# Performance work log

Hardware: AMD Instinct MI355X
Metric: run time of the kernel (lower is better)

Reference implementation:

```python
import jax, jax.numpy as jnp
import numpy as np

EPS = 1e-6
R_DEPTH = 12   # CONFIG['max_recursion_depth']
STACK = 48     # CONFIG['stack_size']
GB, CG, CC = 0.8, 2.0, 0.25  # graph_bias_scale, context_gate_strength, commitment_cost


def _g(k, shape, s=0.05):
    return (jax.random.normal(k, shape) * s).astype(jnp.float32)


def setup_inputs():
    D, V, B, S = 128, 16384, 32, 128
    NS, NM = 64, 128
    ks = iter(jax.random.split(jax.random.key(0), 40))
    return {
        "input_ids": jax.random.randint(next(ks), (B, S), 0, V),
        "prev_syn_idx": jax.random.randint(next(ks), (B,), 0, NS),
        "prev_sem_idx": jax.random.randint(next(ks), (B,), 0, NM),
        "emb_mag": _g(next(ks), (V, D), 1.0),
        "emb_phase": _g(next(ks), (V, D), 1.0),
        "cell_Wr": _g(next(ks), (D, D)), "cell_Wi": _g(next(ks), (D, D)),
        "norm_scale": jnp.ones((D,), jnp.float32),
        "norm_shift": jnp.zeros((D,), jnp.float32),
        "modrelu_b": jnp.zeros((D,), jnp.float32),
        "qWr": _g(next(ks), (D, D)), "qWi": _g(next(ks), (D, D)),
        "kWr": _g(next(ks), (D, D)), "kWi": _g(next(ks), (D, D)),
        "vWr": _g(next(ks), (D, D)), "vWi": _g(next(ks), (D, D)),
        "oWr": _g(next(ks), (D, D)), "oWi": _g(next(ks), (D, D)),
        "halt_W": _g(next(ks), (2 * D, 1)),
        "halt_b": jnp.full((1,), -2.0, jnp.float32),  # nn.init.constant_(halt_linear.bias, -2.0)
        "stk_W": _g(next(ks), (2 * D, 3)), "stk_b": jnp.zeros((3,), jnp.float32),
        "cb_syn": _g(next(ks), (64, 2 * D), 1.0),
        "cb_sem": _g(next(ks), (128, 2 * D), 1.0),
        "ctxsyn_W": _g(next(ks), (2 * D, NS)), "ctxsyn_b": jnp.zeros((NS,), jnp.float32),
        "ctxsem_W": _g(next(ks), (2 * D, NM)), "ctxsem_b": jnp.zeros((NM,), jnp.float32),
        "adj_syn": _g(next(ks), (NS, NS), 1.0),
        "adj_sem": _g(next(ks), (NM, NM), 1.0),
        "gate_W": _g(next(ks), (4 * D, D)), "gate_b": jnp.zeros((D,), jnp.float32),
        "dec_W": _g(next(ks), (2 * D, V)), "dec_b": jnp.zeros((V,), jnp.float32),
    }


def _forward(fl, input_ids, prev_syn_idx, prev_sem_idx):
    (emb_mag, emb_phase, cell_Wr, cell_Wi, norm_scale, norm_shift, modrelu_b,
     qWr, qWi, kWr, kWi, vWr, vWi, oWr, oWi, halt_W, halt_b, stk_W, stk_b,
     cb_syn, cb_sem, ctxsyn_W, ctxsyn_b, ctxsem_W, ctxsem_b, adj_syn, adj_sem,
     gate_W, gate_b, dec_W, dec_b) = fl
    B = input_ids.shape[0]
    D = emb_mag.shape[1]
    sg = jax.lax.stop_gradient

    def clin(r, i, Wr, Wi):  # ComplexLinear (no bias)
        return r @ Wr - i @ Wi, i @ Wr + r @ Wi

    def cell(zr, zi):  # AdaptiveRecursiveCell
        r, i = clin(zr, zi, cell_Wr, cell_Wi)
        # ComplexLayerNorm (torch.var is unbiased -> ddof=1)
        mag = jnp.sqrt(r * r + i * i) + EPS
        mean = mag.mean(-1, keepdims=True)
        var = jnp.var(mag, axis=-1, ddof=1, keepdims=True)
        nm = (mag - mean) / jnp.sqrt(var + EPS) * norm_scale + norm_shift
        r, i = nm * r / mag, nm * i / mag  # cos/sin of original phase
        # ModReLU
        n = jnp.sqrt(r * r + i * i) + EPS
        s = jax.nn.relu(n + modrelu_b) / n
        r, i = r * s, i * s
        # MultiHeadComplexAttention: source computes Q,K but out = V -> o_proj(v_proj(z))
        vr, vi = clin(r, i, vWr, vWi)
        r, i = clin(vr, vi, oWr, oWi)
        zf = jnp.concatenate([r, i], -1)
        halt = jax.nn.sigmoid(zf @ halt_W + halt_b)          # [B,1]
        ctrl = jax.nn.softmax(zf @ stk_W + stk_b, axis=-1)   # [B,3]
        return r, i, halt, ctrl

    def stack_step(zr, zi, mem, ptr, ctrl):  # DifferentiableStack
        push, pop, noop = ctrl[:, 0:1], ctrl[:, 1:2], ctrl[:, 2:3]
        pu, pd = jnp.roll(ptr, 1, axis=1), jnp.roll(ptr, -1, axis=1)
        nptr = push * pu + pop * pd + noop * ptr
        nptr = nptr / (nptr.sum(1, keepdims=True) + EPS)
        zf = jnp.concatenate([zr, zi], -1)
        wm = (push * pu)[:, :, None]                          # write mask [B,STACK,1]
        mem = wm * zf[:, None, :] + mem * (1.0 - wm)
        read = (mem * nptr[:, :, None]).sum(1)                # [B,2D]
        return read[:, :D], read[:, D:], mem, nptr

    def gres(zr, zi, sr, si):  # GatedResidual, g_c = g + i*g
        g = jax.nn.sigmoid(jnp.concatenate([zr, zi, sr, si], -1) @ gate_W + gate_b)
        return ((1.0 - g) * zr + g * zi + g * (sr - si),
                (1.0 - g) * zi - g * zr + g * (si + sr))

    def vq(zr, zi, cb, adj, cW, cbias, pidx):  # ContextAwareDualVQ.vq_step (eval mode)
        zf = jnp.concatenate([zr, zi], -1)                    # [B,2D]
        d = (zf * zf).sum(1, keepdims=True) + (cb * cb).sum(1) - 2.0 * zf @ cb.T
        d = d - GB * jax.nn.sigmoid(adj[pidx]) - CG * jax.nn.softmax(zf @ cW + cbias, -1)
        idx = jnp.argmin(d, axis=1)
        zq = cb[idx]
        loss = jnp.mean((sg(zq) - zf) ** 2) + CC * jnp.mean((zq - sg(zf)) ** 2)
        return zf + sg(zq - zf), loss, idx                    # STE

    def step(carry, ids_t):
        mem, ptr, psyn, psem, lacc = carry
        r, th = emb_mag[ids_t], emb_phase[ids_t]              # embed
        zr, zi = r * jnp.cos(th), r * jnp.sin(th)
        rem = jnp.ones((B, 1), zr.dtype)
        accr = jnp.zeros_like(zr); acci = jnp.zeros_like(zi)
        slr = jnp.zeros_like(zr); sli = jnp.zeros_like(zi)
        for n in range(R_DEPTH):  # ACT recursion, halting-weighted accumulation
            pr, pi, halt, ctrl = cell(zr, zi)
            rr, ri, mem, ptr = stack_step(pr, pi, mem, ptr, ctrl)
            zr, zi = gres(pr, pi, rr, ri)
            w = rem if n == R_DEPTH - 1 else rem * halt
            accr, acci = accr + w * zr, acci + w * zi
            rem = rem * (1.0 - halt)
            slr, sli = slr + zr / R_DEPTH, sli + zi / R_DEPTH
        zqs, ls, isyn = vq(accr, acci, cb_syn, adj_syn, ctxsyn_W, ctxsyn_b, psyn)
        zqm, lm, isem = vq(slr, sli, cb_sem, adj_sem, ctxsem_W, ctxsem_b, psem)
        logits = 0.5 * (zqs + zqm) @ dec_W + dec_b            # decoder: Linear(2D, V)
        return (mem, ptr, isyn, isem, lacc + ls + lm), logits

    mem0 = jnp.zeros((B, STACK, 2 * D), jnp.float32)
    ptr0 = jnp.zeros((B, STACK), jnp.float32).at[:, 0].set(1.0)
    carry0 = (mem0, ptr0, prev_syn_idx, prev_sem_idx, jnp.zeros((), jnp.float32))
    (_, _, _, _, vq_loss), logits = jax.lax.scan(step, carry0, input_ids.T)
    return jnp.transpose(logits, (1, 0, 2)), vq_loss          # [B,S,V], scalar


def reference(input_ids, prev_syn_idx, prev_sem_idx, emb_mag, emb_phase, cell_Wr, cell_Wi, norm_scale, norm_shift, modrelu_b, qWr, qWi, kWr, kWi, vWr, vWi, oWr, oWi, halt_W, halt_b, stk_W, stk_b, cb_syn, cb_sem, ctxsyn_W, ctxsyn_b, ctxsem_W, ctxsem_b, adj_syn, adj_sem, gate_W, gate_b, dec_W, dec_b):
    fl = (emb_mag, emb_phase, cell_Wr, cell_Wi, norm_scale, norm_shift, modrelu_b,
          qWr, qWi, kWr, kWi, vWr, vWi, oWr, oWi, halt_W, halt_b, stk_W, stk_b,
          cb_syn, cb_sem, ctxsyn_W, ctxsyn_b, ctxsem_W, ctxsem_b, adj_syn, adj_sem,
          gate_W, gate_b, dec_W, dec_b)
    return _forward(fl, input_ids, prev_syn_idx, prev_sem_idx)
```

## Files before the change

### kernel.cpp

```cpp
#include <hip/hip_runtime.h>
#include <math.h>

#define D 128
#define D2 256
#define STK 48
#define SEQ 128
#define BATCH 32
#define RDPT 12
#define NSYN 64
#define NSEM 128
#define VOC 16384
#define EPSF 1e-6f
#define GB_C 0.8f
#define CG_C 2.0f

struct RParams {
  const int* input_ids;
  const int* prev_syn;
  const int* prev_sem;
  const float* emb_mag;
  const float* emb_phase;
  const float* cell_Wr;
  const float* cell_Wi;
  const float* norm_scale;
  const float* norm_shift;
  const float* modrelu_b;
  const float* VOr;
  const float* VOi;
  const float* halt_W;
  const float* halt_b;
  const float* stk_W;
  const float* stk_b;
  const float* cb_syn;
  const float* cb_sem;
  const float* ctxsyn_W;
  const float* ctxsyn_b;
  const float* ctxsem_W;
  const float* ctxsem_b;
  const float* gate_W;
  const float* gate_b;
  const float* cbT_syn;
  const float* cbT_sem;
  const float* cnrm_syn;
  const float* cnrm_sem;
  const float* gbsig_syn;
  const float* gbsig_sem;
  float* X;
  float* lossp;
};

__device__ __forceinline__ float waveAllSum(float v) {
  #pragma unroll
  for (int m = 32; m; m >>= 1) v += __shfl_xor(v, m);
  return v;
}

__global__ __launch_bounds__(512, 2) void recur_kernel(RParams p) {
  __shared__ float2 VO2[D * D];
  __shared__ float partr[512], parti[512];
  __shared__ alignas(16) float xr_[D], xi_[D], cr_[D], ci_[D];
  __shared__ float rAiA[D2], marr[D];
  __shared__ alignas(16) float zfc[D2], rd_[D2];
  __shared__ alignas(16) float acc2[D2], sl2[D2];
  __shared__ float zqs[D2];
  __shared__ float sptr[STK];
  __shared__ alignas(16) float nptrs[STK], wms[STK];
  __shared__ float scal[16];
  __shared__ int icb[2];
  __shared__ int ids[SEQ];

  const int tid = threadIdx.x;
  const int b = blockIdx.x;
  const int wv = tid >> 6;
  const int l = tid & 63;
  const int j = tid & 127;
  const int kq = tid >> 7;
  const int k0 = kq * 32;

  float cwr[32], cwi[32];
  #pragma unroll
  for (int kk = 0; kk < 32; ++kk) {
    cwr[kk] = p.cell_Wr[(size_t)(k0 + kk) * D + j];
    cwi[kk] = p.cell_Wi[(size_t)(k0 + kk) * D + j];
  }
  float gw[128];
  #pragma unroll
  for (int kk = 0; kk < 128; ++kk)
    gw[kk] = p.gate_W[(size_t)(kq * 128 + kk) * D + j];
  {
    const float4* r4p = (const float4*)p.VOr;
    const float4* i4p = (const float4*)p.VOi;
    float4* dst = (float4*)VO2;
    for (int e = tid; e < D * D / 4; e += 512) {
      float4 r4 = r4p[e];
      float4 i4 = i4p[e];
      float4 lo, hi;
      lo.x = r4.x; lo.y = i4.x; lo.z = r4.y; lo.w = i4.y;
      hi.x = r4.z; hi.y = i4.z; hi.z = r4.w; hi.w = i4.w;
      dst[e * 2 + 0] = lo;
      dst[e * 2 + 1] = hi;
    }
  }
  float snsR = 0.f, nshR = 0.f, smbR = 0.f, sgbR = 0.f;
  if (tid < D) {
    snsR = p.norm_scale[tid];
    nshR = p.norm_shift[tid];
    smbR = p.modrelu_b[tid];
    sgbR = p.gate_b[tid];
  }
  float hwr0 = 0.f, hwr1 = 0.f, hwr2 = 0.f, hwr3 = 0.f;
  if (wv == 0) {
    hwr0 = p.halt_W[l]; hwr1 = p.halt_W[l + 64];
    hwr2 = p.halt_W[l + 128]; hwr3 = p.halt_W[l + 192];
  } else if (wv < 4) {
    const int c = wv - 1;
    hwr0 = p.stk_W[l * 3 + c]; hwr1 = p.stk_W[(l + 64) * 3 + c];
    hwr2 = p.stk_W[(l + 128) * 3 + c]; hwr3 = p.stk_W[(l + 192) * 3 + c];
  }
  if (tid < SEQ) ids[tid] = p.input_ids[(size_t)b * SEQ + tid];
  if (tid < STK) sptr[tid] = (tid == 0) ? 1.f : 0.f;
  if (tid == 0) { icb[0] = p.prev_syn[b]; icb[1] = p.prev_sem[b]; }
  const float hb = p.halt_b[0];
  const float sb0 = p.stk_b[0], sb1 = p.stk_b[1], sb2 = p.stk_b[2];

  float memv[24];
  #pragma unroll
  for (int q = 0; q < 24; ++q) memv[q] = 0.f;
  const int mdl = tid & 255, mjh = tid >> 8;
  float lossAcc = 0.f;
  __syncthreads();

  for (int t = 0; t < SEQ; ++t) {
    const int id = ids[t];
    if (tid < D) {
      float m = p.emb_mag[(size_t)id * D + tid];
      float ph = p.emb_phase[(size_t)id * D + tid];
      float sv, cv;
      sincosf(ph, &sv, &cv);
      xr_[tid] = m * cv;
      xi_[tid] = m * sv;
    }
    float remv = 1.f;
    float accR = 0.f, accI = 0.f, slR = 0.f, slI = 0.f;
    __syncthreads();

    for (int n = 0; n < RDPT; ++n) {
      {
        const float4* x4r = (const float4*)(&xr_[k0]);
        const float4* x4i = (const float4*)(&xi_[k0]);
        float a0 = 0.f, a1 = 0.f, a2 = 0.f, a3 = 0.f;
        #pragma unroll
        for (int q = 0; q < 8; ++q) {
          float4 xa = x4r[q];
          float4 xb = x4i[q];
          a0 = fmaf(xa.x, cwr[q*4+0], a0); a0 = fmaf(-xb.x, cwi[q*4+0], a0);
          a1 = fmaf(xb.x, cwr[q*4+0], a1); a1 = fmaf(xa.x, cwi[q*4+0], a1);
          a2 = fmaf(xa.y, cwr[q*4+1], a2); a2 = fmaf(-xb.y, cwi[q*4+1], a2);
          a3 = fmaf(xb.y, cwr[q*4+1], a3); a3 = fmaf(xa.y, cwi[q*4+1], a3);
          a0 = fmaf(xa.z, cwr[q*4+2], a0); a0 = fmaf(-xb.z, cwi[q*4+2], a0);
          a1 = fmaf(xb.z, cwr[q*4+2], a1); a1 = fmaf(xa.z, cwi[q*4+2], a1);
          a2 = fmaf(xa.w, cwr[q*4+3], a2); a2 = fmaf(-xb.w, cwi[q*4+3], a2);
          a3 = fmaf(xb.w, cwr[q*4+3], a3); a3 = fmaf(xa.w, cwi[q*4+3], a3);
        }
        partr[tid] = a0 + a2;
        parti[tid] = a1 + a3;
      }
      __syncthreads();
      if (tid < D) {
        float rr = partr[tid] + partr[tid + 128] + partr[tid + 256] + partr[tid + 384];
        float ii = parti[tid] + parti[tid + 128] + parti[tid + 256] + parti[tid + 384];
        rAiA[tid] = rr;
        rAiA[tid + 128] = ii;
        marr[tid] = sqrtf(rr * rr + ii * ii) + EPSF;
      }
      __syncthreads();
      if (tid < 64) {
        float m0 = marr[l], m1 = marr[l + 64];
        float s = waveAllSum(m0 + m1);
        float mean = s * (1.f / D);
        float d0 = m0 - mean, d1 = m1 - mean;
        float v = waveAllSum(d0 * d0 + d1 * d1);
        if (l == 0) {
          scal[1] = mean;
          scal[2] = rsqrtf(v * (1.f / (D - 1)) + EPSF);
        }
      }
      __syncthreads();
      if (tid < D) {
        float m = marr[tid];
        float nm = (m - scal[1]) * scal[2] * snsR + nshR;
        float r_ = nm * rAiA[tid] / m;
        float i_ = nm * rAiA[tid + 128] / m;
        float nn = sqrtf(r_ * r_ + i_ * i_) + EPSF;
        float sc = fmaxf(nn + smbR, 0.f) / nn;
        cr_[tid] = r_ * sc;
        ci_[tid] = i_ * sc;
      }
      __syncthreads();
      {
        const float4* c4r = (const float4*)(&cr_[k0]);
        const float4* c4i = (const float4*)(&ci_[k0]);
        float a0 = 0.f, a1 = 0.f, a2 = 0.f, a3 = 0.f;
        #pragma unroll
        for (int q = 0; q < 8; ++q) {
          float4 xa = c4r[q];
          float4 xb = c4i[q];
          const int kb = k0 + q * 4;
          float2 w0 = VO2[(size_t)(kb + 0) * D + j];
          float2 w1 = VO2[(size_t)(kb + 1) * D + j];
          float2 w2 = VO2[(size_t)(kb + 2) * D + j];
          float2 w3 = VO2[(size_t)(kb + 3) * D + j];
          a0 = fmaf(xa.x, w0.x, a0); a0 = fmaf(-xb.x, w0.y, a0);
          a1 = fmaf(xb.x, w0.x, a1); a1 = fmaf(xa.x, w0.y, a1);
          a2 = fmaf(xa.y, w1.x, a2); a2 = fmaf(-xb.y, w1.y, a2);
          a3 = fmaf(xb.y, w1.x, a3); a3 = fmaf(xa.y, w1.y, a3);
          a0 = fmaf(xa.z, w2.x, a0); a0 = fmaf(-xb.z, w2.y, a0);
          a1 = fmaf(xb.z, w2.x, a1); a1 = fmaf(xa.z, w2.y, a1);
          a2 = fmaf(xa.w, w3.x, a2); a2 = fmaf(-xb.w, w3.y, a2);
          a3 = fmaf(xb.w, w3.x, a3); a3 = fmaf(xa.w, w3.y, a3);
        }
        partr[tid] = a0 + a2;
        parti[tid] = a1 + a3;
      }
      __syncthreads();
      if (tid < D) {
        zfc[tid] = partr[tid] + partr[tid + 128] + partr[tid + 256] + partr[tid + 384];
        zfc[tid + 128] = parti[tid] + parti[tid + 128] + parti[tid + 256] + parti[tid + 384];
      }
      __syncthreads();
      if (tid < 256) {
        float s = zfc[l] * hwr0 + zfc[l + 64] * hwr1 +
                  zfc[l + 128] * hwr2 + zfc[l + 192] * hwr3;
        s = waveAllSum(s);
        if (l == 0) scal[4 + wv] = s;
      }
      __syncthreads();
      if (tid < 64) {
        float halt = 1.f / (1.f + expf(-(scal[4] + hb)));
        float e0 = scal[5] + sb0, e1 = scal[6] + sb1, e2 = scal[7] + sb2;
        float mx = fmaxf(e0, fmaxf(e1, e2));
        float x0 = expf(e0 - mx), x1 = expf(e1 - mx), x2 = expf(e2 - mx);
        float sm = x0 + x1 + x2;
        float push = x0 / sm, pop = x1 / sm, noop = x2 / sm;
        float wgt = (n == RDPT - 1) ? remv : remv * halt;
        if (l == 0) scal[3] = wgt;
        remv = remv * (1.f - halt);
        float pj = 0.f, pu = 0.f, pd = 0.f;
        if (l < STK) {
          pj = sptr[l];
          pu = sptr[(l + STK - 1) % STK];
          pd = sptr[(l + 1) % STK];
        }
        float np_ = push * pu + pop * pd + noop * pj;
        float wm_ = push * pu;
        float ssum = waveAllSum((l < STK) ? np_ : 0.f);
        float inv = 1.f / (ssum + EPSF);
        if (l < STK) {
          np_ *= inv;
          nptrs[l] = np_;
          sptr[l] = np_;
          wms[l] = wm_;
        }
      }
      __syncthreads();
      {
        const float4* wm4 = (const float4*)wms;
        const float4* np4 = (const float4*)nptrs;
        float zfd = zfc[mdl];
        float accA = 0.f, accB = 0.f;
        #pragma unroll
        for (int m4 = 0; m4 < 6; ++m4) {
          float4 wmv = wm4[mjh * 6 + m4];
          float4 npv = np4[mjh * 6 + m4];
          const int base = m4 * 4;
          memv[base + 0] = wmv.x * zfd + memv[base + 0] * (1.f - wmv.x);
          accA = fmaf(memv[base + 0], npv.x, accA);
          memv[base + 1] = wmv.y * zfd + memv[base + 1] * (1.f - wmv.y);
          accB = fmaf(memv[base + 1], npv.y, accB);
          memv[base + 2] = wmv.z * zfd + memv[base + 2] * (1.f - wmv.z);
          accA = fmaf(memv[base + 2], npv.z, accA);
          memv[base + 3] = wmv.w * zfd + memv[base + 3] * (1.f - wmv.w);
          accB = fmaf(memv[base + 3], npv.w, accB);
        }
        partr[tid] = accA + accB;
      }
      __syncthreads();
      if (tid < D2) rd_[tid] = partr[tid] + partr[tid + 256];
      __syncthreads();
      {
        const float4* src4 = (kq < 2) ? (const float4*)(&zfc[kq * 128])
                                      : (const float4*)(&rd_[(kq - 2) * 128]);
        float g0 = 0.f, g1 = 0.f, g2 = 0.f, g3 = 0.f;
        #pragma unroll
        for (int q = 0; q < 32; ++q) {
          float4 xv = src4[q];
          g0 = fmaf(xv.x, gw[q * 4 + 0], g0);
          g1 = fmaf(xv.y, gw[q * 4 + 1], g1);
          g2 = fmaf(xv.z, gw[q * 4 + 2], g2);
          g3 = fmaf(xv.w, gw[q * 4 + 3], g3);
        }
        partr[tid] = (g0 + g1) + (g2 + g3);
      }
      __syncthreads();
      if (tid < D) {
        float g = partr[tid] + partr[tid + 128] + partr[tid + 256] +
                  partr[tid + 384] + sgbR;
        g = 1.f / (1.f + expf(-g));
        float pr_ = zfc[tid], pi_ = zfc[tid + 128];
        float rr_ = rd_[tid], ri_ = rd_[tid + 128];
        float nzr = (1.f - g) * pr_ + g * pi_ + g * (rr_ - ri_);
        float nzi = (1.f - g) * pi_ - g * pr_ + g * (ri_ + rr_);
        xr_[tid] = nzr;
        xi_[tid] = nzi;
        float wgt = scal[3];
        accR += wgt * nzr;
        accI += wgt * nzi;
        slR += nzr * (1.f / RDPT);
        slI += nzi * (1.f / RDPT);
      }
      __syncthreads();
    }

    if (tid < D) {
      acc2[tid] = accR; acc2[tid + 128] = accI;
      sl2[tid] = slR;  sl2[tid + 128] = slI;
    }
    __syncthreads();

    {
      const int c = tid & 63, ch = tid >> 6;
      const int kb = ch * 32;
      const float* cb = p.cbT_syn + (size_t)kb * 64 + c;
      const float* cw = p.ctxsyn_W + (size_t)kb * 64 + c;
      const float4* a4 = (const float4*)(&acc2[kb]);
      float d0 = 0.f, d1 = 0.f, e0 = 0.f, e1 = 0.f;
      #pragma unroll
      for (int q = 0; q < 8; ++q) {
        float4 zv = a4[q];
        d0 = fmaf(cb[(size_t)(q * 4 + 0) * 64], zv.x, d0);
        e0 = fmaf(cw[(size_t)(q * 4 + 0) * 64], zv.x, e0);
        d1 = fmaf(cb[(size_t)(q * 4 + 1) * 64], zv.y, d1);
        e1 = fmaf(cw[(size_t)(q * 4 + 1) * 64], zv.y, e1);
        d0 = fmaf(cb[(size_t)(q * 4 + 2) * 64], zv.z, d0);
        e0 = fmaf(cw[(size_t)(q * 4 + 2) * 64], zv.z, e0);
        d1 = fmaf(cb[(size_t)(q * 4 + 3) * 64], zv.w, d1);
        e1 = fmaf(cw[(size_t)(q * 4 + 3) * 64], zv.w, e1);
      }
      partr[ch * 64 + c] = d0 + d1;
      parti[ch * 64 + c] = e0 + e1;
    }
    __syncthreads();
    if (tid < 64) {
      float dot = 0.f, e = p.ctxsyn_b[l];
      #pragma unroll
      for (int ch = 0; ch < 8; ++ch) {
        dot += partr[ch * 64 + l];
        e += parti[ch * 64 + l];
      }
      float d = p.cnrm_syn[l] - 2.f * dot;
      float m = e;
      #pragma unroll
      for (int mm = 32; mm; mm >>= 1) m = fmaxf(m, __shfl_xor(m, mm));
      float ex = expf(e - m);
      float s = waveAllSum(ex);
      const int pidx = icb[0];
      float score = d - p.gbsig_syn[(size_t)pidx * 64 + l] - CG_C * (ex / s);
      float bv = score; int bi = l;
      #pragma unroll
      for (int mm = 32; mm; mm >>= 1) {
        float ov = __shfl_xor(bv, mm); int oi = __shfl_xor(bi, mm);
        if (ov < bv || (ov == bv && oi < bi)) { bv = ov; bi = oi; }
      }
      if (l == 0) icb[0] = bi;
    }
    __syncthreads();
    if (tid < D2) {
      const int idx = icb[0];
      float zqv = p.cb_syn[(size_t)idx * D2 + tid];
      float df = zqv - acc2[tid];
      lossAcc += df * df;
      zqs[tid] = zqv;
    }
    {
      const int c = tid & 127, ch = tid >> 7;
      const int kb = ch * 64;
      const float* cb = p.cbT_sem + (size_t)kb * 128 + c;
      const float* cw = p.ctxsem_W + (size_t)kb * 128 + c;
      const float4* a4 = (const float4*)(&sl2[kb]);
      float d0 = 0.f, d1 = 0.f, e0 = 0.f, e1 = 0.f;
      #pragma unroll
      for (int q = 0; q < 16; ++q) {
        float4 zv = a4[q];
        d0 = fmaf(cb[(size_t)(q * 4 + 0) * 128], zv.x, d0);
        e0 = fmaf(cw[(size_t)(q * 4 + 0) * 128], zv.x, e0);
        d1 = fmaf(cb[(size_t)(q * 4 + 1) * 128], zv.y, d1);
        e1 = fmaf(cw[(size_t)(q * 4 + 1) * 128], zv.y, e1);
        d0 = fmaf(cb[(size_t)(q * 4 + 2) * 128], zv.z, d0);
        e0 = fmaf(cw[(size_t)(q * 4 + 2) * 128], zv.z, e0);
        d1 = fmaf(cb[(size_t)(q * 4 + 3) * 128], zv.w, d1);
        e1 = fmaf(cw[(size_t)(q * 4 + 3) * 128], zv.w, e1);
      }
      partr[ch * 128 + c] = d0 + d1;
      parti[ch * 128 + c] = e0 + e1;
    }
    __syncthreads();
    if (tid < 64) {
      float dot0 = 0.f, e0 = p.ctxsem_b[l];
      float dot1 = 0.f, e1 = p.ctxsem_b[l + 64];
      #pragma unroll
      for (int ch = 0; ch < 4; ++ch) {
        dot0 += partr[ch * 128 + l];       e0 += parti[ch * 128 + l];
        dot1 += partr[ch * 128 + l + 64];  e1 += parti[ch * 128 + l + 64];
      }
      float d0 = p.cnrm_sem[l] - 2.f * dot0;
      float d1 = p.cnrm_sem[l + 64] - 2.f * dot1;
      float m = fmaxf(e0, e1);
      #pragma unroll
      for (int mm = 32; mm; mm >>= 1) m = fmaxf(m, __shfl_xor(m, mm));
      float x0 = expf(e0 - m), x1 = expf(e1 - m);
      float s = waveAllSum(x0 + x1);
      const int pidx = icb[1];
      float s0 = d0 - p.gbsig_sem[(size_t)pidx * 128 + l] - CG_C * (x0 / s);
      float s1 = d1 - p.gbsig_sem[(size_t)pidx * 128 + l + 64] - CG_C * (x1 / s);
      float bv = s0; int bi = l;
      if (s1 < bv) { bv = s1; bi = l + 64; }
      #pragma unroll
      for (int mm = 32; mm; mm >>= 1) {
        float ov = __shfl_xor(bv, mm); int oi = __shfl_xor(bi, mm);
        if (ov < bv || (ov == bv && oi < bi)) { bv = ov; bi = oi; }
      }
      if (l == 0) icb[1] = bi;
    }
    __syncthreads();
    if (tid < D2) {
      const int idx = icb[1];
      float zqv = p.cb_sem[(size_t)idx * D2 + tid];
      float df = zqv - sl2[tid];
      lossAcc += df * df;
      p.X[(size_t)(b * SEQ + t) * D2 + tid] = 0.5f * (zqs[tid] + zqv);
    }
    __syncthreads();
  }

  partr[tid] = lossAcc;
  __syncthreads();
  if (tid < 256) partr[tid] += partr[tid + 256];
  __syncthreads();
  if (tid < 128) partr[tid] += partr[tid + 128];
  __syncthreads();
  if (tid < 64) {
    float v = partr[tid] + partr[tid + 64];
    v = waveAllSum(v);
    if (tid == 0) p.lossp[b] = v;
  }
}

__global__ __launch_bounds__(256) void voprod_kernel(const float* __restrict__ vr,
                                                     const float* __restrict__ vi,
                                                     const float* __restrict__ orr,
                                                     const float* __restrict__ oii,
                                                     float* __restrict__ VOr,
                                                     float* __restrict__ VOi) {
  __shared__ float a_r[D], a_i[D];
  const int k = blockIdx.x;
  const int tid = threadIdx.x;
  if (tid < D) { a_r[tid] = vr[k * D + tid]; a_i[tid] = vi[k * D + tid]; }
  __syncthreads();
  const int m = tid & 127;
  const int half = tid >> 7;
  float acc = 0.f;
  if (half == 0) {
    #pragma unroll 8
    for (int jj = 0; jj < D; ++jj)
      acc += a_r[jj] * orr[jj * D + m] - a_i[jj] * oii[jj * D + m];
    VOr[k * D + m] = acc;
  } else {
    #pragma unroll 8
    for (int jj = 0; jj < D; ++jj)
      acc += a_r[jj] * oii[jj * D + m] + a_i[jj] * orr[jj * D + m];
    VOi[k * D + m] = acc;
  }
}

__global__ void vqprep_kernel(const float* __restrict__ cb_syn,
                              const float* __restrict__ cb_sem,
                              const float* __restrict__ adj_syn,
                              const float* __restrict__ adj_sem,
                              float* __restrict__ cbT_syn,
                              float* __restrict__ cbT_sem,
                              float* __restrict__ cnrm_syn,
                              float* __restrict__ cnrm_sem,
                              float* __restrict__ gbsig_syn,
                              float* __restrict__ gbsig_sem) {
  const int tid = blockIdx.x * 256 + threadIdx.x;
  const int nt = gridDim.x * 256;
  for (int e = tid; e < NSYN * D2; e += nt) {
    int c = e / D2, k = e % D2;
    cbT_syn[k * NSYN + c] = cb_syn[e];
  }
  for (int e = tid; e < NSEM * D2; e += nt) {
    int c = e / D2, k = e % D2;
    cbT_sem[k * NSEM + c] = cb_sem[e];
  }
  for (int c = tid; c < NSYN; c += nt) {
    float s = 0.f;
    for (int k = 0; k < D2; ++k) { float v = cb_syn[c * D2 + k]; s += v * v; }
    cnrm_syn[c] = s;
  }
  for (int c = tid; c < NSEM; c += nt) {
    float s = 0.f;
    for (int k = 0; k < D2; ++k) { float v = cb_sem[c * D2 + k]; s += v * v; }
    cnrm_sem[c] = s;
  }
  for (int e = tid; e < NSYN * NSYN; e += nt)
    gbsig_syn[e] = GB_C / (1.f + expf(-adj_syn[e]));
  for (int e = tid; e < NSEM * NSEM; e += nt)
    gbsig_sem[e] = GB_C / (1.f + expf(-adj_sem[e]));
}

__global__ __launch_bounds__(256) void dec_kernel(const float* __restrict__ X,
                                                  const float* __restrict__ W,
                                                  const float* __restrict__ bias,
                                                  float* __restrict__ out) {
  __shared__ float A[32][D2];
  const int tid = threadIdx.x;
  const int bx = blockIdx.x;
  const int by = blockIdx.y;
  const float* xr = X + (size_t)by * 32 * D2;
  #pragma unroll
  for (int s = 0; s < 32; ++s) A[s][tid] = xr[s * D2 + tid];
  __syncthreads();
  const int ty = tid >> 5, tx = tid & 31;
  const int col0 = bx * 128 + tx * 4;
  const int r0 = ty * 4;
  float acc[4][4];
  #pragma unroll
  for (int r = 0; r < 4; ++r) {
    acc[r][0] = 0.f; acc[r][1] = 0.f; acc[r][2] = 0.f; acc[r][3] = 0.f;
  }
  const float* wp = W + col0;
  for (int k = 0; k < D2; k += 4) {
    float4 w0 = *(const float4*)(wp + (size_t)(k + 0) * VOC);
    float4 w1 = *(const float4*)(wp + (size_t)(k + 1) * VOC);
    float4 w2 = *(const float4*)(wp + (size_t)(k + 2) * VOC);
    float4 w3 = *(const float4*)(wp + (size_t)(k + 3) * VOC);
    #pragma unroll
    for (int r = 0; r < 4; ++r) {
      float4 a = *(const float4*)&A[r0 + r][k];
      acc[r][0] += a.x * w0.x + a.y * w1.x + a.z * w2.x + a.w * w3.x;
      acc[r][1] += a.x * w0.y + a.y * w1.y + a.z * w2.y + a.w * w3.y;
      acc[r][2] += a.x * w0.z + a.y * w1.z + a.z * w2.z + a.w * w3.z;
      acc[r][3] += a.x * w0.w + a.y * w1.w + a.z * w2.w + a.w * w3.w;
    }
  }
  float4 bv = *(const float4*)(bias + col0);
  #pragma unroll
  for (int r = 0; r < 4; ++r) {
    float4 o;
    o.x = acc[r][0] + bv.x; o.y = acc[r][1] + bv.y;
    o.z = acc[r][2] + bv.z; o.w = acc[r][3] + bv.w;
    *(float4*)(out + (size_t)(by * 32 + r0 + r) * VOC + col0) = o;
  }
}

__global__ void loss_kernel(const float* __restrict__ lp, float* __restrict__ out) {
  int l = threadIdx.x;
  float v = (l < BATCH) ? lp[l] : 0.f;
  #pragma unroll
  for (int off = 32; off; off >>= 1) v += __shfl_down(v, off);
  if (l == 0) out[0] = v * (1.25f / 8192.f);
}

extern "C" void kernel_launch(void* const* d_in, const int* in_sizes, int n_in,
                              void* d_out, int out_size, void* d_ws,
                              size_t ws_size, hipStream_t stream) {
  float* ws = (float*)d_ws;
  float* X = ws;
  float* lossp = X + 1048576;
  float* VOr = lossp + 64;
  float* VOi = VOr + 16384;
  float* cbT_syn = VOi + 16384;
  float* cbT_sem = cbT_syn + 16384;
  float* cnrm_syn = cbT_sem + 32768;
  float* cnrm_sem = cnrm_syn + 64;
  float* gbsig_syn = cnrm_sem + 128;
  float* gbsig_sem = gbsig_syn + 4096;

  RParams p;
  p.input_ids  = (const int*)d_in[0];
  p.prev_syn   = (const int*)d_in[1];
  p.prev_sem   = (const int*)d_in[2];
  p.emb_mag    = (const float*)d_in[3];
  p.emb_phase  = (const float*)d_in[4];
  p.cell_Wr    = (const float*)d_in[5];
  p.cell_Wi    = (const float*)d_in[6];
  p.norm_scale = (const float*)d_in[7];
  p.norm_shift = (const float*)d_in[8];
  p.modrelu_b  = (const float*)d_in[9];
  p.VOr        = VOr;
  p.VOi        = VOi;
  p.halt_W     = (const float*)d_in[18];
  p.halt_b     = (const float*)d_in[19];
  p.stk_W      = (const float*)d_in[20];
  p.stk_b      = (const float*)d_in[21];
  p.cb_syn     = (const float*)d_in[22];
  p.cb_sem     = (const float*)d_in[23];
  p.ctxsyn_W   = (const float*)d_in[24];
  p.ctxsyn_b   = (const float*)d_in[25];
  p.ctxsem_W   = (const float*)d_in[26];
  p.ctxsem_b   = (const float*)d_in[27];
  p.gate_W     = (const float*)d_in[30];
  p.gate_b     = (const float*)d_in[31];
  const float* dec_W = (const float*)d_in[32];
  const float* dec_b = (const float*)d_in[33];
  p.cbT_syn = cbT_syn;
  p.cbT_sem = cbT_sem;
  p.cnrm_syn = cnrm_syn;
  p.cnrm_sem = cnrm_sem;
  p.gbsig_syn = gbsig_syn;
  p.gbsig_sem = gbsig_sem;
  p.X = X;
  p.lossp = lossp;

  float* out = (float*)d_out;

  voprod_kernel<<<D, 256, 0, stream>>>((const float*)d_in[14], (const float*)d_in[15],
                                       (const float*)d_in[16], (const float*)d_in[17],
                                       VOr, VOi);
  vqprep_kernel<<<64, 256, 0, stream>>>((const float*)d_in[22], (const float*)d_in[23],
                                        (const float*)d_in[28], (const float*)d_in[29],
                                        cbT_syn, cbT_sem, cnrm_syn, cnrm_sem,
                                        gbsig_syn, gbsig_sem);
  recur_kernel<<<BATCH, 512, 0, stream>>>(p);
  dec_kernel<<<dim3(VOC / 128, BATCH * SEQ / 32), 256, 0, stream>>>(X, dec_W,
                                                                    dec_b, out);
  loss_kernel<<<1, 64, 0, stream>>>(lossp, out + (size_t)BATCH * SEQ * VOC);
}
```

Before: 16.74 ms.

## Merge reduction and normalization stages to cut barriers in recurrent loop

Inside the 12-step inner recursion, the cell-output reduction, magnitude statistics and modReLU normalization are folded into one wave-0 stage. The halt and stack projections are now computed by a single wave from shared-memory copies of the weights, which removes several __syncthreads per iteration. The VO weight tile is repacked as float4 pairs so each thread does half as many LDS reads. Embedding rows for the next token are prefetched during the tail of the current step. The cost is that more serial work lands on one wave, so other waves sit idle for longer, and the extra shared arrays increase LDS use.

```diff
diff --git a/kernel.cpp b/kernel.cpp
--- a/kernel.cpp
+++ b/kernel.cpp
@@ -56,22 +56,23 @@
 }
 
 __global__ __launch_bounds__(512, 2) void recur_kernel(RParams p) {
-  __shared__ float2 VO2[D * D];
+  __shared__ float4 VO4[(D / 2) * D];
   __shared__ float partr[512], parti[512];
   __shared__ alignas(16) float xr_[D], xi_[D], cr_[D], ci_[D];
-  __shared__ float rAiA[D2], marr[D];
   __shared__ alignas(16) float zfc[D2], rd_[D2];
   __shared__ alignas(16) float acc2[D2], sl2[D2];
   __shared__ float zqs[D2];
   __shared__ float sptr[STK];
   __shared__ alignas(16) float nptrs[STK], wms[STK];
+  __shared__ float sns_s[D], nsh_s[D], smb_s[D];
+  __shared__ float hW_s[D2];
+  __shared__ float stW_s[D2 * 3];
   __shared__ float scal[16];
   __shared__ int icb[2];
   __shared__ int ids[SEQ];
 
   const int tid = threadIdx.x;
   const int b = blockIdx.x;
-  const int wv = tid >> 6;
   const int l = tid & 63;
   const int j = tid & 127;
   const int kq = tid >> 7;
@@ -87,36 +88,24 @@
   #pragma unroll
   for (int kk = 0; kk < 128; ++kk)
     gw[kk] = p.gate_W[(size_t)(kq * 128 + kk) * D + j];
-  {
-    const float4* r4p = (const float4*)p.VOr;
-    const float4* i4p = (const float4*)p.VOi;
-    float4* dst = (float4*)VO2;
-    for (int e = tid; e < D * D / 4; e += 512) {
-      float4 r4 = r4p[e];
-      float4 i4 = i4p[e];
-      float4 lo, hi;
-      lo.x = r4.x; lo.y = i4.x; lo.z = r4.y; lo.w = i4.y;
-      hi.x = r4.z; hi.y = i4.z; hi.z = r4.w; hi.w = i4.w;
-      dst[e * 2 + 0] = lo;
-      dst[e * 2 + 1] = hi;
-    }
-  }
-  float snsR = 0.f, nshR = 0.f, smbR = 0.f, sgbR = 0.f;
+  for (int e = tid; e < (D / 2) * D; e += 512) {
+    const int kp = e >> 7;
+    const int jj = e & 127;
+    float4 w;
+    w.x = p.VOr[(size_t)(2 * kp) * D + jj];
+    w.y = p.VOi[(size_t)(2 * kp) * D + jj];
+    w.z = p.VOr[(size_t)(2 * kp + 1) * D + jj];
+    w.w = p.VOi[(size_t)(2 * kp + 1) * D + jj];
+    VO4[e] = w;
+  }
   if (tid < D) {
-    snsR = p.norm_scale[tid];
-    nshR = p.norm_shift[tid];
-    smbR = p.modrelu_b[tid];
-    sgbR = p.gate_b[tid];
-  }
-  float hwr0 = 0.f, hwr1 = 0.f, hwr2 = 0.f, hwr3 = 0.f;
-  if (wv == 0) {
-    hwr0 = p.halt_W[l]; hwr1 = p.halt_W[l + 64];
-    hwr2 = p.halt_W[l + 128]; hwr3 = p.halt_W[l + 192];
-  } else if (wv < 4) {
-    const int c = wv - 1;
-    hwr0 = p.stk_W[l * 3 + c]; hwr1 = p.stk_W[(l + 64) * 3 + c];
-    hwr2 = p.stk_W[(l + 128) * 3 + c]; hwr3 = p.stk_W[(l + 192) * 3 + c];
-  }
+    sns_s[tid] = p.norm_scale[tid];
+    nsh_s[tid] = p.norm_shift[tid];
+    smb_s[tid] = p.modrelu_b[tid];
+  }
+  const float sgbR = (tid < D) ? p.gate_b[tid] : 0.f;
+  if (tid < D2) hW_s[tid] = p.halt_W[tid];
+  for (int e = tid; e < D2 * 3; e += 512) stW_s[e] = p.stk_W[e];
   if (tid < SEQ) ids[tid] = p.input_ids[(size_t)b * SEQ + tid];
   if (tid < STK) sptr[tid] = (tid == 0) ? 1.f : 0.f;
   if (tid == 0) { icb[0] = p.prev_syn[b]; icb[1] = p.prev_sem[b]; }
@@ -128,20 +117,25 @@
   for (int q = 0; q < 24; ++q) memv[q] = 0.f;
   const int mdl = tid & 255, mjh = tid >> 8;
   float lossAcc = 0.f;
+  float remv = 1.f;
+  float mNxt = 0.f, pNxt = 0.f;
   __syncthreads();
 
+  if (tid < D) {
+    const int id0 = ids[0];
+    mNxt = p.emb_mag[(size_t)id0 * D + tid];
+    pNxt = p.emb_phase[(size_t)id0 * D + tid];
+  }
+
   for (int t = 0; t < SEQ; ++t) {
-    const int id = ids[t];
     if (tid < D) {
-      float m = p.emb_mag[(size_t)id * D + tid];
-      float ph = p.emb_phase[(size_t)id * D + tid];
       float sv, cv;
-      sincosf(ph, &sv, &cv);
-      xr_[tid] = m * cv;
-      xi_[tid] = m * sv;
-    }
-    float remv = 1.f;
+      sincosf(pNxt, &sv, &cv);
+      xr_[tid] = mNxt * cv;
+      xi_[tid] = mNxt * sv;
+    }
     float accR = 0.f, accI = 0.f, slR = 0.f, slI = 0.f;
+    if (tid < 64) remv = 1.f;
     __syncthreads();
 
     for (int n = 0; n < RDPT; ++n) {
@@ -166,78 +160,80 @@
         parti[tid] = a1 + a3;
       }
       __syncthreads();
-      if (tid < D) {
-        float rr = partr[tid] + partr[tid + 128] + partr[tid + 256] + partr[tid + 384];
-        float ii = parti[tid] + parti[tid + 128] + parti[tid + 256] + parti[tid + 384];
-        rAiA[tid] = rr;
-        rAiA[tid + 128] = ii;
-        marr[tid] = sqrtf(rr * rr + ii * ii) + EPSF;
-      }
-      __syncthreads();
       if (tid < 64) {
-        float m0 = marr[l], m1 = marr[l + 64];
-        float s = waveAllSum(m0 + m1);
-        float mean = s * (1.f / D);
-        float d0 = m0 - mean, d1 = m1 - mean;
-        float v = waveAllSum(d0 * d0 + d1 * d1);
-        if (l == 0) {
-          scal[1] = mean;
-          scal[2] = rsqrtf(v * (1.f / (D - 1)) + EPSF);
-        }
-      }
-      __syncthreads();
-      if (tid < D) {
-        float m = marr[tid];
-        float nm = (m - scal[1]) * scal[2] * snsR + nshR;
-        float r_ = nm * rAiA[tid] / m;
-        float i_ = nm * rAiA[tid + 128] / m;
-        float nn = sqrtf(r_ * r_ + i_ * i_) + EPSF;
-        float sc = fmaxf(nn + smbR, 0.f) / nn;
-        cr_[tid] = r_ * sc;
-        ci_[tid] = i_ * sc;
+        float rr0 = 0.f, ii0 = 0.f, rr1 = 0.f, ii1 = 0.f;
+        #pragma unroll
+        for (int q = 0; q < 4; ++q) {
+          rr0 += partr[l + q * 128];       ii0 += parti[l + q * 128];
+          rr1 += partr[l + 64 + q * 128];  ii1 += parti[l + 64 + q * 128];
+        }
+        float m0 = sqrtf(rr0 * rr0 + ii0 * ii0) + EPSF;
+        float m1 = sqrtf(rr1 * rr1 + ii1 * ii1) + EPSF;
+        float mean = waveAllSum(m0 + m1) * (1.f / D);
+        float dd0 = m0 - mean, dd1 = m1 - mean;
+        float istd = rsqrtf(waveAllSum(dd0 * dd0 + dd1 * dd1) * (1.f / (D - 1)) + EPSF);
+        float nm0 = (m0 - mean) * istd * sns_s[l] + nsh_s[l];
+        float r0_ = nm0 * rr0 / m0, i0_ = nm0 * ii0 / m0;
+        float nn0 = sqrtf(r0_ * r0_ + i0_ * i0_) + EPSF;
+        float sc0 = fmaxf(nn0 + smb_s[l], 0.f) / nn0;
+        cr_[l] = r0_ * sc0;
+        ci_[l] = i0_ * sc0;
+        float nm1 = (m1 - mean) * istd * sns_s[l + 64] + nsh_s[l + 64];
+        float r1_ = nm1 * rr1 / m1, i1_ = nm1 * ii1 / m1;
+        float nn1 = sqrtf(r1_ * r1_ + i1_ * i1_) + EPSF;
+        float sc1 = fmaxf(nn1 + smb_s[l + 64], 0.f) / nn1;
+        cr_[l + 64] = r1_ * sc1;
+        ci_[l + 64] = i1_ * sc1;
       }
       __syncthreads();
       {
         const float4* c4r = (const float4*)(&cr_[k0]);
         const float4* c4i = (const float4*)(&ci_[k0]);
+        const float4* vbase = &VO4[(size_t)(k0 >> 1) * D + j];
         float a0 = 0.f, a1 = 0.f, a2 = 0.f, a3 = 0.f;
         #pragma unroll
         for (int q = 0; q < 8; ++q) {
           float4 xa = c4r[q];
           float4 xb = c4i[q];
-          const int kb = k0 + q * 4;
-          float2 w0 = VO2[(size_t)(kb + 0) * D + j];
-          float2 w1 = VO2[(size_t)(kb + 1) * D + j];
-          float2 w2 = VO2[(size_t)(kb + 2) * D + j];
-          float2 w3 = VO2[(size_t)(kb + 3) * D + j];
-          a0 = fmaf(xa.x, w0.x, a0); a0 = fmaf(-xb.x, w0.y, a0);
-          a1 = fmaf(xb.x, w0.x, a1); a1 = fmaf(xa.x, w0.y, a1);
-          a2 = fmaf(xa.y, w1.x, a2); a2 = fmaf(-xb.y, w1.y, a2);
-          a3 = fmaf(xb.y, w1.x, a3); a3 = fmaf(xa.y, w1.y, a3);
-          a0 = fmaf(xa.z, w2.x, a0); a0 = fmaf(-xb.z, w2.y, a0);
-          a1 = fmaf(xb.z, w2.x, a1); a1 = fmaf(xa.z, w2.y, a1);
-          a2 = fmaf(xa.w, w3.x, a2); a2 = fmaf(-xb.w, w3.y, a2);
-          a3 = fmaf(xb.w, w3.x, a3); a3 = fmaf(xa.w, w3.y, a3);
+          float4 wA = vbase[(size_t)(2 * q) * D];
+          float4 wB = vbase[(size_t)(2 * q + 1) * D];
+          a0 = fmaf(xa.x, wA.x, a0); a0 = fmaf(-xb.x, wA.y, a0);
+          a1 = fmaf(xb.x, wA.x, a1); a1 = fmaf(xa.x, wA.y, a1);
+          a2 = fmaf(xa.y, wA.z, a2); a2 = fmaf(-xb.y, wA.w, a2);
+          a3 = fmaf(xb.y, wA.z, a3); a3 = fmaf(xa.y, wA.w, a3);
+          a0 = fmaf(xa.z, wB.x, a0); a0 = fmaf(-xb.z, wB.y, a0);
+          a1 = fmaf(xb.z, wB.x, a1); a1 = fmaf(xa.z, wB.y, a1);
+          a2 = fmaf(xa.w, wB.z, a2); a2 = fmaf(-xb.w, wB.w, a2);
+          a3 = fmaf(xb.w, wB.z, a3); a3 = fmaf(xa.w, wB.w, a3);
         }
         partr[tid] = a0 + a2;
         parti[tid] = a1 + a3;
       }
       __syncthreads();
-      if (tid < D) {
-        zfc[tid] = partr[tid] + partr[tid + 128] + partr[tid + 256] + partr[tid + 384];
-        zfc[tid + 128] = parti[tid] + parti[tid + 128] + parti[tid + 256] + parti[tid + 384];
-      }
-      __syncthreads();
       if (tid < 256) {
-        float s = zfc[l] * hwr0 + zfc[l + 64] * hwr1 +
-                  zfc[l + 128] * hwr2 + zfc[l + 192] * hwr3;
-        s = waveAllSum(s);
-        if (l == 0) scal[4 + wv] = s;
+        if (tid < 128) {
+          zfc[tid] = partr[tid] + partr[tid + 128] + partr[tid + 256] + partr[tid + 384];
+        } else {
+          const int d = tid - 128;
+          zfc[tid] = parti[d] + parti[d + 128] + parti[d + 256] + parti[d + 384];
+        }
       }
       __syncthreads();
       if (tid < 64) {
-        float halt = 1.f / (1.f + expf(-(scal[4] + hb)));
-        float e0 = scal[5] + sb0, e1 = scal[6] + sb1, e2 = scal[7] + sb2;
+        float z0 = zfc[l], z1 = zfc[l + 64], z2 = zfc[l + 128], z3 = zfc[l + 192];
+        float dh  = z0 * hW_s[l] + z1 * hW_s[l + 64] + z2 * hW_s[l + 128] + z3 * hW_s[l + 192];
+        float dc0 = z0 * stW_s[l * 3 + 0] + z1 * stW_s[(l + 64) * 3 + 0] +
+                    z2 * stW_s[(l + 128) * 3 + 0] + z3 * stW_s[(l + 192) * 3 + 0];
+        float dc1 = z0 * stW_s[l * 3 + 1] + z1 * stW_s[(l + 64) * 3 + 1] +
+                    z2 * stW_s[(l + 128) * 3 + 1] + z3 * stW_s[(l + 192) * 3 + 1];
+        float dc2 = z0 * stW_s[l * 3 + 2] + z1 * stW_s[(l + 64) * 3 + 2] +
+                    z2 * stW_s[(l + 128) * 3 + 2] + z3 * stW_s[(l + 192) * 3 + 2];
+        dh = waveAllSum(dh);
+        dc0 = waveAllSum(dc0);
+        dc1 = waveAllSum(dc1);
+        dc2 = waveAllSum(dc2);
+        float halt = 1.f / (1.f + expf(-(dh + hb)));
+        float e0 = dc0 + sb0, e1 = dc1 + sb1, e2 = dc2 + sb2;
         float mx = fmaxf(e0, fmaxf(e1, e2));
         float x0 = expf(e0 - mx), x1 = expf(e1 - mx), x2 = expf(e2 - mx);
         float sm = x0 + x1 + x2;
@@ -321,6 +317,11 @@
       __syncthreads();
     }
 
+    if (tid < D) {
+      const int idn = ids[(t + 1 < SEQ) ? t + 1 : t];
+      mNxt = p.emb_mag[(size_t)idn * D + tid];
+      pNxt = p.emb_phase[(size_t)idn * D + tid];
+    }
     if (tid < D) {
       acc2[tid] = accR; acc2[tid + 128] = accI;
       sl2[tid] = slR;  sl2[tid + 128] = slI;
```

Result: slower. 18.01 ms (+7.6%).
